# Kernel optimization log

Measured on AMD Instinct MI355X. Metric: run time of the kernel, lower is better.

Reference implementation:

```python
import jax, jax.numpy as jnp
from jax import lax
import numpy as np

B, A, D = 4, 512, 729   # batch, num_angles, detector pixels
H, W = 512, 512         # reconstruction volume


def setup_inputs() -> dict:
    key = jax.random.key(0)
    sino = jax.random.normal(key, (B, A, D), dtype=jnp.float32)
    vol_spacing = np.array([1.0, 1.0], dtype=np.float32)          # (sy, sx)
    det_spacing = np.array([1.0], dtype=np.float32)
    vol_origin = np.array([-(H - 1) / 2.0, -(W - 1) / 2.0], dtype=np.float32)
    det_origin = np.array([-(D - 1) / 2.0], dtype=np.float32)
    angles = jnp.linspace(0.0, jnp.pi, A, endpoint=False, dtype=jnp.float32)
    return {
        "input": sino,
        "volume_shape": np.array([H, W], dtype=np.int64),
        "volume_origin": jnp.asarray(vol_origin),
        "detector_origin": jnp.asarray(det_origin),
        "volume_spacing": jnpp if False else jnp.asarray(vol_spacing),
        "detector_spacing": jnp.asarray(det_spacing),
        "trajectory": angles,
    }


def _backproject(sino, vol_shape, vol_origin, det_origin, vol_spacing, det_spacing, angles):
    h, w = int(vol_shape[0]), int(vol_shape[1])
    d = sino.shape[-1]
    ys = vol_origin[0] + jnp.arange(h, dtype=sino.dtype) * vol_spacing[0]  # [H]
    xs = vol_origin[1] + jnp.arange(w, dtype=sino.dtype) * vol_spacing[1]  # [W]

    def step(acc, per_angle):
        theta, sino_a = per_angle                      # scalar, [B, D]
        # ray coordinate s = x*cos(theta) + y*sin(theta) for every voxel
        s = xs[None, :] * jnp.cos(theta) + ys[:, None] * jnp.sin(theta)  # [H, W]
        u = (s - det_origin[0]) / det_spacing[0]       # continuous detector index
        u0 = jnp.floor(u)
        frac = u - u0
        i0 = u0.astype(jnp.int32)
        i1 = i0 + 1
        valid0 = (i0 >= 0) & (i0 < d)
        valid1 = (i1 >= 0) & (i1 < d)
        i0c = jnp.clip(i0, 0, d - 1)
        i1c = jnp.clip(i1, 0, d - 1)
        v0 = sino_a[:, i0c]                            # [B, H, W] gather
        v1 = sino_a[:, i1c]                            # [B, H, W] gather
        contrib = (jnp.where(valid0, (1.0 - frac) * v0, 0.0)
                   + jnp.where(valid1, frac * v1, 0.0))
        return acc + contrib, None

    acc0 = jnp.zeros((sino.shape[0], h, w), dtype=sino.dtype)
    out, _ = lax.scan(step, acc0, (angles, jnp.swapaxes(sino, 0, 1)))
    return out


def reference(input, volume_shape, volume_origin, detector_origin,
              volume_spacing, detector_spacing, trajectory):
    return _backproject(input, volume_shape, volume_origin, detector_origin,
                        volume_spacing, detector_spacing, trajectory)
```

## Files before the change

### kernel.cpp

```cpp
#include <hip/hip_runtime.h>

#define BB 4
#define AA 512
#define AH 256
#define DD 729
#define HH 512
#define WW 512
#define TSZ 16
#define CH  16
#define WIN 32

typedef float f4v __attribute__((ext_vector_type(4)));

__device__ inline float buf_load1(__amdgpu_buffer_rsrc_t r, int vo) {
    union { unsigned int u; float f; } c;
    c.u = __builtin_amdgcn_raw_buffer_load_b32(r, vo, 0, 0);
    return c.f;
}

__global__ __launch_bounds__(256, 8) void bp_kernel(
    const float* __restrict__ sino,
    const float* __restrict__ vol_origin,
    const float* __restrict__ det_origin,
    const float* __restrict__ vol_spacing,
    const float* __restrict__ det_spacing,
    const float* __restrict__ angles,
    float* __restrict__ out)
{
    __shared__ f4v   s_csk[AH];
    __shared__ float s_win[CH * WIN * BB];

    const int tid = threadIdx.y * TSZ + threadIdx.x;
    const float inv_ds = 1.0f / det_spacing[0];
    const int zh = blockIdx.z;

    const int x0 = blockIdx.x * TSZ;
    const int y0 = blockIdx.y * TSZ;
    const float vsx = vol_spacing[1], vsy = vol_spacing[0];
    const float off = -det_origin[0] * inv_ds;
    const float xc = vol_origin[1] + ((float)x0 + 7.5f) * vsx;
    const float yc = vol_origin[0] + ((float)y0 + 7.5f) * vsy;

    for (int a = tid; a < AH; a += 256) {
        float th = angles[zh * AH + a];
        float c = cosf(th) * inv_ds;
        float s = sinf(th) * inv_ds;
        float uc = fmaf(xc, c, fmaf(yc, s, off));
        int s0 = min(max((int)uc - (WIN / 2), 0), DD - WIN);
        f4v k;
        k.x = c; k.y = s; k.z = off - (float)s0; k.w = __int_as_float(s0);
        s_csk[a] = k;
    }
    __syncthreads();

    const int ix = x0 + threadIdx.x;
    const int iy = y0 + threadIdx.y;
    const float xw = vol_origin[1] + (float)ix * vsx;
    const float yw = vol_origin[0] + (float)iy * vsy;

    const __amdgpu_buffer_rsrc_t rsrc = __builtin_amdgcn_make_buffer_rsrc(
        (void*)sino, (short)0, BB * AA * DD * 4, 0x00020000);

    f4v acc = {0.f, 0.f, 0.f, 0.f};

    for (int a0 = 0; a0 < AH; a0 += CH) {
        #pragma unroll
        for (int k = 0; k < 8; ++k) {
            const int idx = k * 256 + tid;
            const int bb  = idx & 3;
            const int e   = (idx >> 2) & 31;
            const int ja  = idx >> 7;
            const int s0  = __float_as_int(s_csk[a0 + ja].w);
            const int gi  = bb * (AA * DD) + (zh * AH + a0 + ja) * DD + s0 + e;
            s_win[(ja * WIN + e) * BB + bb] = buf_load1(rsrc, gi * 4);
        }
        __syncthreads();

        #pragma unroll 4
        for (int j = 0; j < CH; ++j) {
            const f4v  k  = s_csk[a0 + j];
            const float ul = fmaf(xw, k.x, fmaf(yw, k.y, k.z));
            const int   li = (int)ul;
            const float fr = ul - (float)li;
            const float* w = &s_win[(j * WIN + li) * BB];
            const f4v P = *(const f4v*)(w);
            const f4v Q = *(const f4v*)(w + BB);
            const f4v fr4 = {fr, fr, fr, fr};
            acc = acc + P + fr4 * (Q - P);
        }
        __syncthreads();
    }

    const size_t HW = (size_t)HH * WW;
    const size_t o  = (size_t)iy * WW + ix;
    unsafeAtomicAdd(&out[o],          acc.x);
    unsafeAtomicAdd(&out[o + HW],     acc.y);
    unsafeAtomicAdd(&out[o + 2 * HW], acc.z);
    unsafeAtomicAdd(&out[o + 3 * HW], acc.w);
}

extern "C" void kernel_launch(void* const* d_in, const int* in_sizes, int n_in,
                              void* d_out, int out_size, void* d_ws, size_t ws_size,
                              hipStream_t stream) {
    const float* sino        = (const float*)d_in[0];
    const float* vol_origin  = (const float*)d_in[2];
    const float* det_origin  = (const float*)d_in[3];
    const float* vol_spacing = (const float*)d_in[4];
    const float* det_spacing = (const float*)d_in[5];
    const float* angles      = (const float*)d_in[6];
    float* out = (float*)d_out;

    hipMemsetAsync(d_out, 0, (size_t)out_size * sizeof(float), stream);

    dim3 block(TSZ, TSZ, 1);
    dim3 grid(WW / TSZ, HH / TSZ, 2);
    bp_kernel<<<grid, block, 0, stream>>>(sino, vol_origin, det_origin,
                                          vol_spacing, det_spacing, angles, out);
}
```

Measured before the change: 141.4 us.

## Compute two voxels per thread, load sinogram windows via global_load_lds, split angles four ways

Each thread now handles two voxels eight rows apart within a 16x16 tile, using 128-thread blocks. The second voxel's detector coordinate comes from the first by adding a precomputed offset, which halves the per-angle coordinate math and s_csk reads per voxel. Sinogram windows are copied straight into LDS with global_load_lds instead of going through registers. The angle range is split into four z-slices instead of two, raising block count at the cost of twice as many output atomics.

```diff
diff --git a/kernel.cpp b/kernel.cpp
--- a/kernel.cpp
+++ b/kernel.cpp
@@ -2,23 +2,23 @@
 
 #define BB 4
 #define AA 512
-#define AH 256
+#define ZS 4
+#define AH (AA / ZS)
 #define DD 729
 #define HH 512
 #define WW 512
-#define TSZ 16
-#define CH  16
+#define CH 16
 #define WIN 32
 
 typedef float f4v __attribute__((ext_vector_type(4)));
 
-__device__ inline float buf_load1(__amdgpu_buffer_rsrc_t r, int vo) {
-    union { unsigned int u; float f; } c;
-    c.u = __builtin_amdgcn_raw_buffer_load_b32(r, vo, 0, 0);
-    return c.f;
+__device__ inline void gload_lds(const float* g, float* l) {
+    __builtin_amdgcn_global_load_lds(
+        (const __attribute__((address_space(1))) unsigned int*)g,
+        (__attribute__((address_space(3))) unsigned int*)l, 4, 0, 0);
 }
 
-__global__ __launch_bounds__(256, 8) void bp_kernel(
+__global__ __launch_bounds__(128, 8) void bp_kernel(
     const float* __restrict__ sino,
     const float* __restrict__ vol_origin,
     const float* __restrict__ det_origin,
@@ -28,75 +28,94 @@
     float* __restrict__ out)
 {
     __shared__ f4v   s_csk[AH];
+    __shared__ int   s_s0[AH];
     __shared__ float s_win[CH * WIN * BB];
 
-    const int tid = threadIdx.y * TSZ + threadIdx.x;
+    const int tid  = threadIdx.y * 16 + threadIdx.x;
+    const int lane = tid & 63;
+    const int wv   = tid >> 6;
+
     const float inv_ds = 1.0f / det_spacing[0];
-    const int zh = blockIdx.z;
+    const int abase = blockIdx.z * AH;
 
-    const int x0 = blockIdx.x * TSZ;
-    const int y0 = blockIdx.y * TSZ;
+    const int x0 = blockIdx.x * 16;
+    const int y0 = blockIdx.y * 16;
     const float vsx = vol_spacing[1], vsy = vol_spacing[0];
     const float off = -det_origin[0] * inv_ds;
     const float xc = vol_origin[1] + ((float)x0 + 7.5f) * vsx;
     const float yc = vol_origin[0] + ((float)y0 + 7.5f) * vsy;
 
-    for (int a = tid; a < AH; a += 256) {
-        float th = angles[zh * AH + a];
+    for (int a = tid; a < AH; a += 128) {
+        float th = angles[abase + a];
         float c = cosf(th) * inv_ds;
         float s = sinf(th) * inv_ds;
         float uc = fmaf(xc, c, fmaf(yc, s, off));
         int s0 = min(max((int)uc - (WIN / 2), 0), DD - WIN);
         f4v k;
-        k.x = c; k.y = s; k.z = off - (float)s0; k.w = __int_as_float(s0);
+        k.x = c; k.y = s; k.z = off - (float)s0; k.w = 8.0f * vsy * s;
         s_csk[a] = k;
+        s_s0[a]  = s0;
     }
     __syncthreads();
 
-    const int ix = x0 + threadIdx.x;
-    const int iy = y0 + threadIdx.y;
+    const int ix  = x0 + threadIdx.x;
+    const int iyA = y0 + threadIdx.y;
     const float xw = vol_origin[1] + (float)ix * vsx;
-    const float yw = vol_origin[0] + (float)iy * vsy;
+    const float yw = vol_origin[0] + (float)iyA * vsy;
 
-    const __amdgpu_buffer_rsrc_t rsrc = __builtin_amdgcn_make_buffer_rsrc(
-        (void*)sino, (short)0, BB * AA * DD * 4, 0x00020000);
+    const int sidx = wv * 64 + lane;
+    const int se   = sidx >> 2;
+    const int sbb  = lane & 3;
+    const long sgoff = (long)sbb * (AA * DD) + se;
 
-    f4v acc = {0.f, 0.f, 0.f, 0.f};
+    f4v accA = {0.f, 0.f, 0.f, 0.f};
+    f4v accB = {0.f, 0.f, 0.f, 0.f};
 
     for (int a0 = 0; a0 < AH; a0 += CH) {
         #pragma unroll
-        for (int k = 0; k < 8; ++k) {
-            const int idx = k * 256 + tid;
-            const int bb  = idx & 3;
-            const int e   = (idx >> 2) & 31;
-            const int ja  = idx >> 7;
-            const int s0  = __float_as_int(s_csk[a0 + ja].w);
-            const int gi  = bb * (AA * DD) + (zh * AH + a0 + ja) * DD + s0 + e;
-            s_win[(ja * WIN + e) * BB + bb] = buf_load1(rsrc, gi * 4);
+        for (int i = 0; i < CH; ++i) {
+            const int  s0  = s_s0[a0 + i];
+            const long row = (long)(abase + a0 + i) * DD + s0;
+            gload_lds(sino + row + sgoff, &s_win[i * (WIN * BB) + wv * 64]);
         }
         __syncthreads();
 
-        #pragma unroll 4
+        #pragma unroll
         for (int j = 0; j < CH; ++j) {
             const f4v  k  = s_csk[a0 + j];
-            const float ul = fmaf(xw, k.x, fmaf(yw, k.y, k.z));
-            const int   li = (int)ul;
-            const float fr = ul - (float)li;
-            const float* w = &s_win[(j * WIN + li) * BB];
-            const f4v P = *(const f4v*)(w);
-            const f4v Q = *(const f4v*)(w + BB);
-            const f4v fr4 = {fr, fr, fr, fr};
-            acc = acc + P + fr4 * (Q - P);
+            const float u0 = fmaf(xw, k.x, fmaf(yw, k.y, k.z));
+            const float u1 = u0 + k.w;
+            {
+                const int   li = (int)u0;
+                const float fr = __builtin_amdgcn_fractf(u0);
+                const f4v* w = (const f4v*)&s_win[(j * WIN + li) * BB];
+                const f4v P = w[0], Q = w[1];
+                const f4v fr4 = {fr, fr, fr, fr};
+                accA = accA + P + fr4 * (Q - P);
+            }
+            {
+                const int   li = (int)u1;
+                const float fr = __builtin_amdgcn_fractf(u1);
+                const f4v* w = (const f4v*)&s_win[(j * WIN + li) * BB];
+                const f4v P = w[0], Q = w[1];
+                const f4v fr4 = {fr, fr, fr, fr};
+                accB = accB + P + fr4 * (Q - P);
+            }
         }
         __syncthreads();
     }
 
     const size_t HW = (size_t)HH * WW;
-    const size_t o  = (size_t)iy * WW + ix;
-    unsafeAtomicAdd(&out[o],          acc.x);
-    unsafeAtomicAdd(&out[o + HW],     acc.y);
-    unsafeAtomicAdd(&out[o + 2 * HW], acc.z);
-    unsafeAtomicAdd(&out[o + 3 * HW], acc.w);
+    const size_t oA = (size_t)iyA * WW + ix;
+    const size_t oB = oA + (size_t)8 * WW;
+    unsafeAtomicAdd(&out[oA],          accA.x);
+    unsafeAtomicAdd(&out[oA + HW],     accA.y);
+    unsafeAtomicAdd(&out[oA + 2 * HW], accA.z);
+    unsafeAtomicAdd(&out[oA + 3 * HW], accA.w);
+    unsafeAtomicAdd(&out[oB],          accB.x);
+    unsafeAtomicAdd(&out[oB + HW],     accB.y);
+    unsafeAtomicAdd(&out[oB + 2 * HW], accB.z);
+    unsafeAtomicAdd(&out[oB + 3 * HW], accB.w);
 }
 
 extern "C" void kernel_launch(void* const* d_in, const int* in_sizes, int n_in,
@@ -112,8 +131,8 @@
 
     hipMemsetAsync(d_out, 0, (size_t)out_size * sizeof(float), stream);
 
-    dim3 block(TSZ, TSZ, 1);
-    dim3 grid(WW / TSZ, HH / TSZ, 2);
+    dim3 block(16, 8, 1);
+    dim3 grid(WW / 16, HH / 16, ZS);
     bp_kernel<<<grid, block, 0, stream>>>(sino, vol_origin, det_origin,
                                           vol_spacing, det_spacing, angles, out);
 }
```

New measurement: 142.8 us. About the same (+1.0%).
